# Performance work log

Measured on AMD Instinct MI355X. Metric: run time of the kernel, lower is better.

The kernel has to match this reference:

```python
import jax, jax.numpy as jnp
import numpy as np

B, T, D = 2, 2048, 1024
G, E, F = 4, 4, 4096          # num_groups, experts_per_group, d_ff
KG, KE = 2, 1                  # top_k_groups, top_k_experts


def setup_inputs() -> dict:
    key = jax.random.key(0)
    ks = jax.random.split(key, 5)
    init = lambda k, shape, fan: jax.random.normal(k, shape, jnp.float32) / np.sqrt(fan).astype(np.float32)
    x = jax.random.normal(ks[0], (B, T, D), jnp.float32)
    Wg = init(ks[1], (G, D), D)          # group router (torch Linear weight [out,in])
    We = init(ks[2], (G, E, D), D)       # per-group expert routers
    W1 = init(ks[3], (G, E, F, D), D)    # expert up-proj weights
    W2 = init(ks[4], (G, E, D, F), F)    # expert down-proj weights
    return {"x": x, "Wg": Wg, "We": We, "W1": W1, "W2": W2}


def _moe_forward(x, Wg, We, W1, W2):
    b, t, d = x.shape
    xf = x.reshape(b * t, d)                                   # [N, D]
    group_logits = xf @ Wg.T                                   # [N, G]
    gw, gid = jax.lax.top_k(group_logits, KG)                  # [N, KG]
    gw = jax.nn.softmax(gw, axis=-1)
    expert_logits = jnp.einsum('nd,ged->nge', xf, We)          # [N, G, E]
    sel = jnp.take_along_axis(expert_logits, gid[:, :, None], axis=1)  # [N, KG, E]
    ew, eid = jax.lax.top_k(sel, KE)                           # [N, KG, KE]
    ew = jax.nn.softmax(ew, axis=-1)
    w = gw[:, :, None] * ew                                    # [N, KG, KE]
    oh_g = jax.nn.one_hot(gid, G, dtype=xf.dtype)              # [N, KG, G]
    oh_e = jax.nn.one_hot(eid, E, dtype=xf.dtype)              # [N, KG, KE, E]
    # topk group ids are distinct, and expert ids within a group are distinct,
    # so this scatter-by-one-hot exactly reproduces the masked accumulation.
    combine = jnp.einsum('nrg,nrke,nrk->nge', oh_g, oh_e, w)   # [N, G, E]
    out = jnp.zeros_like(xf)
    for g in range(G):
        for e in range(E):
            h = jax.nn.gelu(xf @ W1[g, e].T, approximate=False)  # exact GELU, as nn.GELU()
            out = out + combine[:, g, e, None] * (h @ W2[g, e].T)
    return out.reshape(b, t, d), group_logits.reshape(b, t, G)


def reference(x, Wg, We, W1, W2):
    out, group_logits = _moe_forward(x, Wg, We, W1, W2)
    p = jax.nn.softmax(group_logits, axis=-1)
    lp = jax.nn.log_softmax(group_logits, axis=-1)
    group_entropy = -(p * lp).sum(-1).mean()
    return out, group_logits, group_entropy
```

## Files before the change

### kernel.cpp

```cpp
#include <hip/hip_runtime.h>
#include <hip/hip_bf16.h>

#define NTOK 4096
#define DDIM 1024
#define GG 4
#define EE 4
#define FF 4096
#define NEXP 16
#define OUT_ELEMS 4194304
#define GL_OFF 4194304
#define ENT_OFF 4210688

typedef float f32x4 __attribute__((ext_vector_type(4)));
typedef short short8 __attribute__((ext_vector_type(8)));

__device__ inline unsigned short f2bf(float f) {
  unsigned int u = __float_as_uint(f);
  unsigned int rounding = 0x7FFFu + ((u >> 16) & 1u);
  return (unsigned short)((u + rounding) >> 16);
}
__device__ inline unsigned int pack2(float f0, float f1) {
  return (unsigned int)f2bf(f0) | ((unsigned int)f2bf(f1) << 16);
}
__device__ inline unsigned int pack2rn(float f0, float f1) {
  unsigned int u0 = __float_as_uint(f0), u1 = __float_as_uint(f1);
  return ((u0 + 0x8000u) >> 16) | ((u1 + 0x8000u) & 0xFFFF0000u);
}

__device__ __forceinline__ void gload_lds16(const void* g, void* l) {
  __builtin_amdgcn_global_load_lds(
      (const __attribute__((address_space(1))) unsigned int*)g,
      (__attribute__((address_space(3))) unsigned int*)l, 16, 0, 0);
}

__global__ void cvt_kernel(const float* __restrict__ x, unsigned short* __restrict__ xb) {
  int idx = blockIdx.x * 256 + threadIdx.x;
  const float4* p = reinterpret_cast<const float4*>(x) + (size_t)idx * 2;
  float4 a = p[0], b = p[1];
  uint4 v;
  v.x = pack2(a.x, a.y); v.y = pack2(a.z, a.w);
  v.z = pack2(b.x, b.y); v.w = pack2(b.z, b.w);
  reinterpret_cast<uint4*>(xb)[idx] = v;
}

__global__ __launch_bounds__(256) void routing_kernel(
    const float* __restrict__ x, const float* __restrict__ Wg,
    const float* __restrict__ We, float* __restrict__ out,
    int* __restrict__ cnt, int* __restrict__ tokL, int* __restrict__ hrwL,
    float* __restrict__ wslot) {
  int wave = threadIdx.x >> 6, lane = threadIdx.x & 63;
  int token = blockIdx.x * 4 + wave;
  const float4* xr = reinterpret_cast<const float4*>(x + (size_t)token * DDIM);
  float4 xv[4];
#pragma unroll
  for (int c = 0; c < 4; c++) xv[c] = xr[c * 64 + lane];

  auto dotrow = [&](const float* w) -> float {
    const float4* w4 = reinterpret_cast<const float4*>(w);
    float s = 0.f;
#pragma unroll
    for (int c = 0; c < 4; c++) {
      float4 wv = w4[c * 64 + lane];
      s += xv[c].x * wv.x + xv[c].y * wv.y + xv[c].z * wv.z + xv[c].w * wv.w;
    }
#pragma unroll
    for (int off = 32; off; off >>= 1) s += __shfl_xor(s, off, 64);
    return s;
  };

  float gl[GG];
#pragma unroll
  for (int g = 0; g < GG; g++) gl[g] = dotrow(Wg + g * DDIM);

  int g0 = 0;
  for (int g = 1; g < GG; g++) if (gl[g] > gl[g0]) g0 = g;
  int g1 = -1;
  for (int g = 0; g < GG; g++) { if (g == g0) continue; if (g1 < 0 || gl[g] > gl[g1]) g1 = g; }
  float e1 = __expf(gl[g1] - gl[g0]);
  float inv = 1.f / (1.f + e1);
  float w0 = inv, w1 = e1 * inv;

  int gsel[2] = {g0, g1};
  float wsel[2] = {w0, w1};
  int esel[2];
#pragma unroll
  for (int r = 0; r < 2; r++) {
    float el[EE];
#pragma unroll
    for (int e = 0; e < EE; e++) el[e] = dotrow(We + ((size_t)gsel[r] * EE + e) * DDIM);
    int best = 0;
    for (int e = 1; e < EE; e++) if (el[e] > el[best]) best = e;
    esel[r] = best;
  }

  float m = gl[0];
  for (int g = 1; g < GG; g++) m = fmaxf(m, gl[g]);
  float se = 0.f;
  for (int g = 0; g < GG; g++) se += __expf(gl[g] - m);
  float lse = __logf(se);
  float ent = 0.f;
  for (int g = 0; g < GG; g++) {
    float lp = gl[g] - m - lse;
    ent -= __expf(lp) * lp;
  }

  if (lane == 0) {
    for (int g = 0; g < GG; g++) out[GL_OFF + token * GG + g] = gl[g];
    atomicAdd(out + ENT_OFF, ent * (1.0f / NTOK));
    for (int r = 0; r < 2; r++) {
      int ge = gsel[r] * EE + esel[r];
      int pos = atomicAdd(cnt + ge, 1);
      tokL[ge * NTOK + pos] = token;
      hrwL[ge * NTOK + pos] = r * NTOK + token;
      wslot[r * NTOK + token] = wsel[r];
    }
  }
}

template <int KDIM, bool UP>
__global__ __launch_bounds__(512, 4) void moe_gemm(
    const unsigned short* __restrict__ A, const float* __restrict__ W,
    const int* __restrict__ cnt, const int* __restrict__ tokL,
    const int* __restrict__ hrwL, unsigned short* __restrict__ Hout,
    float* __restrict__ Yout) {
  constexpr int NT = KDIM / 64;
  constexpr int NROWS = UP ? FF : DDIM;
  int ge = blockIdx.z, mt = blockIdx.y;
  int count = cnt[ge];
  if (mt * 128 >= count) return;
  int n0 = blockIdx.x * 128;

  __shared__ alignas(16) unsigned short As[2][128 * 64];
  __shared__ alignas(16) unsigned short Bs[2][128 * 64];
  __shared__ int srcS[128];
  __shared__ int dstS[128];

  int t = threadIdx.x;
  int w = t >> 6, lane = t & 63;
  if (t < 128) {
    int i = mt * 128 + t;
    bool valid = i < count;
    int hrw = valid ? hrwL[ge * NTOK + i] : -1;
    dstS[t] = hrw;
    if (UP) srcS[t] = valid ? tokL[ge * NTOK + i] : 0;
    else    srcS[t] = hrw < 0 ? 0 : hrw;
  }
  __syncthreads();

  int rA = w * 16 + (lane >> 3);
  int cA = (lane & 7) ^ (lane >> 3);
  const unsigned short* gA0 = A + (size_t)srcS[rA] * KDIM + cA * 8;
  const unsigned short* gA1 = A + (size_t)srcS[rA + 8] * KDIM + cA * 8;

  int rB = t >> 3;
  int cB = t & 7;
  const float* gB0 = W + ((size_t)ge * NROWS + n0 + rB) * KDIM + cB * 8;
  const float* gB1 = W + ((size_t)ge * NROWS + n0 + 64 + rB) * KDIM + cB * 8;
  int pB = (cB ^ (rB & 7)) * 8;

  int wr = w >> 1, wc = w & 1;
  int m0 = wr * 32, nw = wc * 64;
  int rl = lane & 15, kq = lane >> 4;
  int xr = rl & 7;

  f32x4 acc[2][4] = {};
  int cur = 0;

  {
    gload_lds16(gA0, &As[0][(w * 16) * 64]);
    gload_lds16(gA1, &As[0][(w * 16 + 8) * 64]);
    float4 q0 = *reinterpret_cast<const float4*>(gB0);
    float4 q1 = *reinterpret_cast<const float4*>(gB0 + 4);
    float4 q2 = *reinterpret_cast<const float4*>(gB1);
    float4 q3 = *reinterpret_cast<const float4*>(gB1 + 4);
    uint4 v0, v1;
    v0.x = pack2rn(q0.x, q0.y); v0.y = pack2rn(q0.z, q0.w);
    v0.z = pack2rn(q1.x, q1.y); v0.w = pack2rn(q1.z, q1.w);
    v1.x = pack2rn(q2.x, q2.y); v1.y = pack2rn(q2.z, q2.w);
    v1.z = pack2rn(q3.x, q3.y); v1.w = pack2rn(q3.z, q3.w);
    *reinterpret_cast<uint4*>(&Bs[0][rB * 64 + pB]) = v0;
    *reinterpret_cast<uint4*>(&Bs[0][(rB + 64) * 64 + pB]) = v1;
  }
  __syncthreads();

  for (int it = 0; it < NT; ++it) {
    int kb = (it + 1) * 64;
    bool pre = (it + 1) < NT;
    float4 q0, q1, q2, q3;
    if (pre) {
      gload_lds16(gA0 + kb, &As[cur ^ 1][(w * 16) * 64]);
      gload_lds16(gA1 + kb, &As[cur ^ 1][(w * 16 + 8) * 64]);
      q0 = *reinterpret_cast<const float4*>(gB0 + kb);
      q1 = *reinterpret_cast<const float4*>(gB0 + kb + 4);
      q2 = *reinterpret_cast<const float4*>(gB1 + kb);
      q3 = *reinterpret_cast<const float4*>(gB1 + kb + 4);
    }
    const unsigned short* Ab = As[cur];
    const unsigned short* Bb = Bs[cur];
#pragma unroll
    for (int kk = 0; kk < 2; kk++) {
      int cph = ((kk * 4 + kq) ^ xr) * 8;
      short8 af0 = *reinterpret_cast<const short8*>(&Ab[(m0 + rl) * 64 + cph]);
      short8 af1 = *reinterpret_cast<const short8*>(&Ab[(m0 + 16 + rl) * 64 + cph]);
#pragma unroll
      for (int j = 0; j < 4; j++) {
        short8 bf = *reinterpret_cast<const short8*>(&Bb[(nw + j * 16 + rl) * 64 + cph]);
        acc[0][j] = __builtin_amdgcn_mfma_f32_16x16x32_bf16(af0, bf, acc[0][j], 0, 0, 0);
        acc[1][j] = __builtin_amdgcn_mfma_f32_16x16x32_bf16(af1, bf, acc[1][j], 0, 0, 0);
      }
    }
    if (pre) {
      uint4 v0, v1;
      v0.x = pack2rn(q0.x, q0.y); v0.y = pack2rn(q0.z, q0.w);
      v0.z = pack2rn(q1.x, q1.y); v0.w = pack2rn(q1.z, q1.w);
      v1.x = pack2rn(q2.x, q2.y); v1.y = pack2rn(q2.z, q2.w);
      v1.z = pack2rn(q3.x, q3.y); v1.w = pack2rn(q3.z, q3.w);
      *reinterpret_cast<uint4*>(&Bs[cur ^ 1][rB * 64 + pB]) = v0;
      *reinterpret_cast<uint4*>(&Bs[cur ^ 1][(rB + 64) * 64 + pB]) = v1;
    }
    __syncthreads();
    cur ^= 1;
  }

  int re = kq * 4;
#pragma unroll
  for (int i = 0; i < 2; i++) {
#pragma unroll
    for (int e = 0; e < 4; e++) {
      int hr = dstS[m0 + i * 16 + re + e];
      if (hr >= 0) {
        if constexpr (UP) {
#pragma unroll
          for (int j = 0; j < 4; j++) {
            float v = acc[i][j][e];
            float gel = 0.5f * v * (1.0f + erff(v * 0.70710678118654752f));
            Hout[(size_t)hr * FF + n0 + nw + j * 16 + rl] = f2bf(gel);
          }
        } else {
#pragma unroll
          for (int j = 0; j < 4; j++)
            Yout[(size_t)hr * DDIM + n0 + nw + j * 16 + rl] = acc[i][j][e];
        }
      }
    }
  }
}

__global__ void combine_kernel(const float* __restrict__ Y,
                               const float* __restrict__ wslot,
                               float* __restrict__ out) {
  int idx = blockIdx.x * 256 + threadIdx.x;
  int token = idx >> 8;
  float w0 = wslot[token], w1 = wslot[NTOK + token];
  float4 a = reinterpret_cast<const float4*>(Y)[idx];
  float4 b = reinterpret_cast<const float4*>(Y + (size_t)NTOK * DDIM)[idx];
  float4 o;
  o.x = w0 * a.x + w1 * b.x;
  o.y = w0 * a.y + w1 * b.y;
  o.z = w0 * a.z + w1 * b.z;
  o.w = w0 * a.w + w1 * b.w;
  reinterpret_cast<float4*>(out)[idx] = o;
}

extern "C" void kernel_launch(void* const* d_in, const int* in_sizes, int n_in,
                              void* d_out, int out_size, void* d_ws, size_t ws_size,
                              hipStream_t stream) {
  const float* x  = (const float*)d_in[0];
  const float* Wg = (const float*)d_in[1];
  const float* We = (const float*)d_in[2];
  const float* W1 = (const float*)d_in[3];
  const float* W2 = (const float*)d_in[4];
  float* out = (float*)d_out;
  char* ws = (char*)d_ws;

  int* cnt = (int*)(ws);
  int* tokL = (int*)(ws + 1024);
  int* hrwL = (int*)(ws + 1024 + 262144);
  float* wslot = (float*)(ws + 1024 + 524288);
  unsigned short* xb = (unsigned short*)(ws + (1 << 20));
  unsigned short* H  = (unsigned short*)(ws + (1 << 20) + 8388608);
  float* Y = (float*)(ws + (1 << 20) + 8388608 + 67108864);

  hipMemsetAsync(d_out, 0, (size_t)out_size * sizeof(float), stream);
  hipMemsetAsync(ws, 0, 1024, stream);

  cvt_kernel<<<2048, 256, 0, stream>>>(x, xb);
  routing_kernel<<<1024, 256, 0, stream>>>(x, Wg, We, out, cnt, tokL, hrwL, wslot);
  moe_gemm<DDIM, true><<<dim3(FF / 128, 32, NEXP), 512, 0, stream>>>(
      xb, W1, cnt, tokL, hrwL, H, nullptr);
  moe_gemm<FF, false><<<dim3(DDIM / 128, 32, NEXP), 512, 0, stream>>>(
      H, W2, cnt, tokL, hrwL, nullptr, Y);
  combine_kernel<<<4096, 256, 0, stream>>>(Y, wslot, out);
}
```

Baseline: 915.9 us.

## Compact expert tile grid, widen per-wave MFMA tile, fuse bf16 cast into routing

The GEMM grid changes from a sparse 32×16 per-expert layout, where most blocks exit early, to a compacted list of up to 80 tiles mapped through a prefix scan over expert counts. Blocks drop from 512 to 256 threads, and each wave now computes a 64×64 tile with 16 accumulators, so every LDS fragment is reused more often. The separate x→bf16 conversion kernel is folded into the routing kernel, and the entropy atomic is replaced by per-block partial sums plus a one-block finalize kernel. This adds register pressure and a serial scan over expert counts in every block, and it assumes the total tile count fits in 80.

```diff
diff --git a/kernel.cpp b/kernel.cpp
--- a/kernel.cpp
+++ b/kernel.cpp
@@ -7,6 +7,7 @@
 #define EE 4
 #define FF 4096
 #define NEXP 16
+#define MAXTILES 80
 #define OUT_ELEMS 4194304
 #define GL_OFF 4194304
 #define ENT_OFF 4210688
@@ -33,27 +34,29 @@
       (__attribute__((address_space(3))) unsigned int*)l, 16, 0, 0);
 }
 
-__global__ void cvt_kernel(const float* __restrict__ x, unsigned short* __restrict__ xb) {
-  int idx = blockIdx.x * 256 + threadIdx.x;
-  const float4* p = reinterpret_cast<const float4*>(x) + (size_t)idx * 2;
-  float4 a = p[0], b = p[1];
-  uint4 v;
-  v.x = pack2(a.x, a.y); v.y = pack2(a.z, a.w);
-  v.z = pack2(b.x, b.y); v.w = pack2(b.z, b.w);
-  reinterpret_cast<uint4*>(xb)[idx] = v;
-}
-
 __global__ __launch_bounds__(256) void routing_kernel(
     const float* __restrict__ x, const float* __restrict__ Wg,
     const float* __restrict__ We, float* __restrict__ out,
     int* __restrict__ cnt, int* __restrict__ tokL, int* __restrict__ hrwL,
-    float* __restrict__ wslot) {
+    float* __restrict__ wslot, unsigned short* __restrict__ xb,
+    float* __restrict__ entPart) {
   int wave = threadIdx.x >> 6, lane = threadIdx.x & 63;
   int token = blockIdx.x * 4 + wave;
   const float4* xr = reinterpret_cast<const float4*>(x + (size_t)token * DDIM);
   float4 xv[4];
 #pragma unroll
   for (int c = 0; c < 4; c++) xv[c] = xr[c * 64 + lane];
+
+  {
+    uint2* xbr = reinterpret_cast<uint2*>(xb + (size_t)token * DDIM);
+#pragma unroll
+    for (int c = 0; c < 4; c++) {
+      uint2 pv;
+      pv.x = pack2(xv[c].x, xv[c].y);
+      pv.y = pack2(xv[c].z, xv[c].w);
+      xbr[c * 64 + lane] = pv;
+    }
+  }
 
   auto dotrow = [&](const float* w) -> float {
     const float4* w4 = reinterpret_cast<const float4*>(w);
@@ -104,9 +107,10 @@
     ent -= __expf(lp) * lp;
   }
 
+  __shared__ float entS[4];
   if (lane == 0) {
+    entS[wave] = ent;
     for (int g = 0; g < GG; g++) out[GL_OFF + token * GG + g] = gl[g];
-    atomicAdd(out + ENT_OFF, ent * (1.0f / NTOK));
     for (int r = 0; r < 2; r++) {
       int ge = gsel[r] * EE + esel[r];
       int pos = atomicAdd(cnt + ge, 1);
@@ -115,19 +119,43 @@
       wslot[r * NTOK + token] = wsel[r];
     }
   }
+  __syncthreads();
+  if (threadIdx.x == 0)
+    entPart[blockIdx.x] = entS[0] + entS[1] + entS[2] + entS[3];
+}
+
+__global__ void ent_finalize(const float* __restrict__ entPart,
+                             float* __restrict__ out) {
+  int t = threadIdx.x;
+  float s = 0.f;
+  for (int i = t; i < 1024; i += 256) s += entPart[i];
+#pragma unroll
+  for (int off = 32; off; off >>= 1) s += __shfl_xor(s, off, 64);
+  __shared__ float ws4[4];
+  if ((t & 63) == 0) ws4[t >> 6] = s;
+  __syncthreads();
+  if (t == 0) out[ENT_OFF] = (ws4[0] + ws4[1] + ws4[2] + ws4[3]) * (1.0f / NTOK);
 }
 
 template <int KDIM, bool UP>
-__global__ __launch_bounds__(512, 4) void moe_gemm(
+__global__ __launch_bounds__(256, 2) void moe_gemm(
     const unsigned short* __restrict__ A, const float* __restrict__ W,
     const int* __restrict__ cnt, const int* __restrict__ tokL,
     const int* __restrict__ hrwL, unsigned short* __restrict__ Hout,
     float* __restrict__ Yout) {
   constexpr int NT = KDIM / 64;
   constexpr int NROWS = UP ? FF : DDIM;
-  int ge = blockIdx.z, mt = blockIdx.y;
+  int ge = -1, mt = 0;
+  {
+    int y = blockIdx.y, a = 0;
+    for (int g = 0; g < NEXP; g++) {
+      int ntl = (cnt[g] + 127) >> 7;
+      if (y < a + ntl) { ge = g; mt = y - a; break; }
+      a += ntl;
+    }
+  }
+  if (ge < 0) return;
   int count = cnt[ge];
-  if (mt * 128 >= count) return;
   int n0 = blockIdx.x * 128;
 
   __shared__ alignas(16) unsigned short As[2][128 * 64];
@@ -147,76 +175,87 @@
   }
   __syncthreads();
 
-  int rA = w * 16 + (lane >> 3);
   int cA = (lane & 7) ^ (lane >> 3);
-  const unsigned short* gA0 = A + (size_t)srcS[rA] * KDIM + cA * 8;
-  const unsigned short* gA1 = A + (size_t)srcS[rA + 8] * KDIM + cA * 8;
-
-  int rB = t >> 3;
-  int cB = t & 7;
-  const float* gB0 = W + ((size_t)ge * NROWS + n0 + rB) * KDIM + cB * 8;
-  const float* gB1 = W + ((size_t)ge * NROWS + n0 + 64 + rB) * KDIM + cB * 8;
+  const unsigned short* gA[4];
+#pragma unroll
+  for (int c = 0; c < 4; c++)
+    gA[c] = A + (size_t)srcS[w * 32 + c * 8 + (lane >> 3)] * KDIM + cA * 8;
+
+  int rB = t >> 3, cB = t & 7;
+  const float* gB = W + ((size_t)ge * NROWS + n0 + rB) * KDIM + cB * 8;
   int pB = (cB ^ (rB & 7)) * 8;
 
   int wr = w >> 1, wc = w & 1;
-  int m0 = wr * 32, nw = wc * 64;
+  int m0 = wr * 64, nw = wc * 64;
   int rl = lane & 15, kq = lane >> 4;
   int xr = rl & 7;
 
-  f32x4 acc[2][4] = {};
+  f32x4 acc[4][4] = {};
   int cur = 0;
 
   {
-    gload_lds16(gA0, &As[0][(w * 16) * 64]);
-    gload_lds16(gA1, &As[0][(w * 16 + 8) * 64]);
-    float4 q0 = *reinterpret_cast<const float4*>(gB0);
-    float4 q1 = *reinterpret_cast<const float4*>(gB0 + 4);
-    float4 q2 = *reinterpret_cast<const float4*>(gB1);
-    float4 q3 = *reinterpret_cast<const float4*>(gB1 + 4);
-    uint4 v0, v1;
-    v0.x = pack2rn(q0.x, q0.y); v0.y = pack2rn(q0.z, q0.w);
-    v0.z = pack2rn(q1.x, q1.y); v0.w = pack2rn(q1.z, q1.w);
-    v1.x = pack2rn(q2.x, q2.y); v1.y = pack2rn(q2.z, q2.w);
-    v1.z = pack2rn(q3.x, q3.y); v1.w = pack2rn(q3.z, q3.w);
-    *reinterpret_cast<uint4*>(&Bs[0][rB * 64 + pB]) = v0;
-    *reinterpret_cast<uint4*>(&Bs[0][(rB + 64) * 64 + pB]) = v1;
+    float4 q[8];
+#pragma unroll
+    for (int qq = 0; qq < 4; qq++) {
+      q[qq * 2]     = *reinterpret_cast<const float4*>(gB + (size_t)(qq * 32) * KDIM);
+      q[qq * 2 + 1] = *reinterpret_cast<const float4*>(gB + (size_t)(qq * 32) * KDIM + 4);
+    }
+#pragma unroll
+    for (int c = 0; c < 4; c++)
+      gload_lds16(gA[c], &As[0][(w * 32 + c * 8) * 64]);
+#pragma unroll
+    for (int qq = 0; qq < 4; qq++) {
+      uint4 v;
+      v.x = pack2rn(q[qq * 2].x, q[qq * 2].y);
+      v.y = pack2rn(q[qq * 2].z, q[qq * 2].w);
+      v.z = pack2rn(q[qq * 2 + 1].x, q[qq * 2 + 1].y);
+      v.w = pack2rn(q[qq * 2 + 1].z, q[qq * 2 + 1].w);
+      *reinterpret_cast<uint4*>(&Bs[0][(rB + qq * 32) * 64 + pB]) = v;
+    }
   }
   __syncthreads();
 
   for (int it = 0; it < NT; ++it) {
     int kb = (it + 1) * 64;
     bool pre = (it + 1) < NT;
-    float4 q0, q1, q2, q3;
+    float4 q[8];
     if (pre) {
-      gload_lds16(gA0 + kb, &As[cur ^ 1][(w * 16) * 64]);
-      gload_lds16(gA1 + kb, &As[cur ^ 1][(w * 16 + 8) * 64]);
-      q0 = *reinterpret_cast<const float4*>(gB0 + kb);
-      q1 = *reinterpret_cast<const float4*>(gB0 + kb + 4);
-      q2 = *reinterpret_cast<const float4*>(gB1 + kb);
-      q3 = *reinterpret_cast<const float4*>(gB1 + kb + 4);
+#pragma unroll
+      for (int qq = 0; qq < 4; qq++) {
+        q[qq * 2]     = *reinterpret_cast<const float4*>(gB + (size_t)(qq * 32) * KDIM + kb);
+        q[qq * 2 + 1] = *reinterpret_cast<const float4*>(gB + (size_t)(qq * 32) * KDIM + kb + 4);
+      }
+#pragma unroll
+      for (int c = 0; c < 4; c++)
+        gload_lds16(gA[c] + kb, &As[cur ^ 1][(w * 32 + c * 8) * 64]);
     }
     const unsigned short* Ab = As[cur];
     const unsigned short* Bb = Bs[cur];
 #pragma unroll
     for (int kk = 0; kk < 2; kk++) {
       int cph = ((kk * 4 + kq) ^ xr) * 8;
-      short8 af0 = *reinterpret_cast<const short8*>(&Ab[(m0 + rl) * 64 + cph]);
-      short8 af1 = *reinterpret_cast<const short8*>(&Ab[(m0 + 16 + rl) * 64 + cph]);
+      short8 af[4];
+#pragma unroll
+      for (int i = 0; i < 4; i++)
+        af[i] = *reinterpret_cast<const short8*>(&Ab[(m0 + i * 16 + rl) * 64 + cph]);
 #pragma unroll
       for (int j = 0; j < 4; j++) {
         short8 bf = *reinterpret_cast<const short8*>(&Bb[(nw + j * 16 + rl) * 64 + cph]);
-        acc[0][j] = __builtin_amdgcn_mfma_f32_16x16x32_bf16(af0, bf, acc[0][j], 0, 0, 0);
-        acc[1][j] = __builtin_amdgcn_mfma_f32_16x16x32_bf16(af1, bf, acc[1][j], 0, 0, 0);
+#pragma unroll
+        for (int i = 0; i < 4; i++)
+          acc[i][j] = __builtin_amdgcn_mfma_f32_16x16x32_bf16(af[i], bf, acc[i][j], 0, 0, 0);
       }
     }
     if (pre) {
-      uint4 v0, v1;
-      v0.x = pack2rn(q0.x, q0.y); v0.y = pack2rn(q0.z, q0.w);
-      v0.z = pack2rn(q1.x, q1.y); v0.w = pack2rn(q1.z, q1.w);
-      v1.x = pack2rn(q2.x, q2.y); v1.y = pack2rn(q2.z, q2.w);
-      v1.z = pack2rn(q3.x, q3.y); v1.w = pack2rn(q3.z, q3.w);
-      *reinterpret_cast<uint4*>(&Bs[cur ^ 1][rB * 64 + pB]) = v0;
-      *reinterpret_cast<uint4*>(&Bs[cur ^ 1][(rB + 64) * 64 + pB]) = v1;
+#pragma unroll
+      for (int qq = 0; qq < 4; qq++) {
+        uint4 v;
+        v.x = pack2rn(q[qq * 2].x, q[qq * 2].y);
+        v.y = pack2rn(q[qq * 2].z, q[qq * 2].w);
+        v.z = pack2rn(q[qq * 2 + 1].x, q[qq * 2 + 1].y);
+        v.w = pack2rn(q[qq * 2 + 1].z, q[qq * 2 + 1].w);
+        *reinterpret_cast<uint4*>(&Bs[cur ^ 1][(rB + qq * 32) * 64 + pB]) = v;
+      }
     }
     __syncthreads();
     cur ^= 1;
@@ -224,7 +263,7 @@
 
   int re = kq * 4;
 #pragma unroll
-  for (int i = 0; i < 2; i++) {
+  for (int i = 0; i < 4; i++) {
 #pragma unroll
     for (int e = 0; e < 4; e++) {
       int hr = dstS[m0 + i * 16 + re + e];
@@ -277,6 +316,7 @@
   int* tokL = (int*)(ws + 1024);
   int* hrwL = (int*)(ws + 1024 + 262144);
   float* wslot = (float*)(ws + 1024 + 524288);
+  float* entPart = (float*)(ws + 1024 + 524288 + 32768);
   unsigned short* xb = (unsigned short*)(ws + (1 << 20));
   unsigned short* H  = (unsigned short*)(ws + (1 << 20) + 8388608);
   float* Y = (float*)(ws + (1 << 20) + 8388608 + 67108864);
@@ -284,11 +324,12 @@
   hipMemsetAsync(d_out, 0, (size_t)out_size * sizeof(float), stream);
   hipMemsetAsync(ws, 0, 1024, stream);
 
-  cvt_kernel<<<2048, 256, 0, stream>>>(x, xb);
-  routing_kernel<<<1024, 256, 0, stream>>>(x, Wg, We, out, cnt, tokL, hrwL, wslot);
-  moe_gemm<DDIM, true><<<dim3(FF / 128, 32, NEXP), 512, 0, stream>>>(
+  routing_kernel<<<1024, 256, 0, stream>>>(x, Wg, We, out, cnt, tokL, hrwL,
+                                           wslot, xb, entPart);
+  moe_gemm<DDIM, true><<<dim3(FF / 128, MAXTILES), 256, 0, stream>>>(
       xb, W1, cnt, tokL, hrwL, H, nullptr);
-  moe_gemm<FF, false><<<dim3(DDIM / 128, 32, NEXP), 512, 0, stream>>>(
+  moe_gemm<FF, false><<<dim3(DDIM / 128, MAXTILES), 256, 0, stream>>>(
       H, W2, cnt, tokL, hrwL, nullptr, Y);
   combine_kernel<<<4096, 256, 0, stream>>>(Y, wslot, out);
-}
+  ent_finalize<<<1, 256, 0, stream>>>(entPart, out);
+}
```

Result: slower. 1.032 ms (+12.7%).
